# Kernel optimization log

Hardware: AMD Instinct MI355X
Metric: run time of the kernel (lower is better)

Reference implementation:

```python
import jax, jax.numpy as jnp
import numpy as np

IN_FEATURES = 4096
OUT_FEATURES = 4096
TOKENS = 8192


def setup_inputs() -> dict:
    key = jax.random.key(0)
    kx, kw, kb = jax.random.split(key, 3)
    x = jax.random.normal(kx, (TOKENS, IN_FEATURES), dtype=jnp.float32)
    # Simulate the offline quantization: a float weight quantized to 2-bit signed {-2,-1,0,1}
    w_f = jax.random.normal(kw, (OUT_FEATURES, IN_FEATURES), dtype=jnp.float32) * 0.02
    max_val = jnp.max(jnp.abs(w_f))
    scale = (max_val / 1.5 + 1e-8).astype(jnp.float32)
    weight_q = jnp.clip(jnp.round(w_f / scale), -2, 1).astype(jnp.int8)
    bias = jax.random.normal(kb, (OUT_FEATURES,), dtype=jnp.float32) * 0.01
    return {"x": x, "weight_q": weight_q, "scale": scale, "bias": bias}


def reference(x, weight_q, scale, bias):
    # Dequantize 2-bit weights then standard linear: y = x @ W^T + b
    w = weight_q.astype(jnp.float32) * scale  # [out, in]
    return jnp.einsum('ti,oi->to', x, w) + bias
```

## Files before the change

### kernel.cpp

```cpp
#include <hip/hip_runtime.h>
#include <stdint.h>

#define TOKENS 8192
#define INF    4096
#define OUTF   4096
#define NT     64

typedef __bf16 bf16x8 __attribute__((ext_vector_type(8)));
typedef float  f32x4  __attribute__((ext_vector_type(4)));
typedef unsigned short ushort_t;

__device__ __forceinline__ unsigned short f2bf(float f) {
  union { float f; unsigned int u; } v;
  v.f = f;
  unsigned int r = v.u + 0x7fffu + ((v.u >> 16) & 1u);
  return (unsigned short)(r >> 16);
}

__global__ void l2b_conv_x(const float* __restrict__ x,
                           unsigned short* __restrict__ xb, int n4) {
  int idx = blockIdx.x * blockDim.x + threadIdx.x;
  int stride = gridDim.x * blockDim.x;
  for (int i = idx; i < n4; i += stride) {
    float4 v = reinterpret_cast<const float4*>(x)[i];
    ushort4 o;
    o.x = f2bf(v.x); o.y = f2bf(v.y); o.z = f2bf(v.z); o.w = f2bf(v.w);
    reinterpret_cast<ushort4*>(xb)[i] = o;
  }
}

__global__ void l2b_conv_w(const int* __restrict__ w,
                           unsigned short* __restrict__ wb, int n4) {
  int idx = blockIdx.x * blockDim.x + threadIdx.x;
  int stride = gridDim.x * blockDim.x;
  for (int i = idx; i < n4; i += stride) {
    int4 v = reinterpret_cast<const int4*>(w)[i];
    ushort4 o;
    o.x = f2bf((float)v.x); o.y = f2bf((float)v.y);
    o.z = f2bf((float)v.z); o.w = f2bf((float)v.w);
    reinterpret_cast<ushort4*>(wb)[i] = o;
  }
}

__device__ __forceinline__ void gload_lds16(const ushort_t* g, ushort_t* l) {
  auto gp = reinterpret_cast<__attribute__((address_space(1))) unsigned int*>(
      reinterpret_cast<uintptr_t>(g));
  auto lp = reinterpret_cast<__attribute__((address_space(3))) unsigned int*>(
      reinterpret_cast<uintptr_t>(l));
  __builtin_amdgcn_global_load_lds(gp, lp, 16, 0, 0);
}

__device__ __forceinline__ bf16x8 ldsRd(const ushort_t* slot, int row, int chunk) {
  const int off = (row << 7) + ((chunk ^ (row & 7)) << 4);
  return *reinterpret_cast<const bf16x8*>(
      reinterpret_cast<const char*>(slot) + off);
}

__device__ __forceinline__ void stage_half(const ushort_t* __restrict__ src,
                                           ushort_t* slot, int wid,
                                           int ge0, int ge1) {
  gload_lds16(src + ge0, slot + wid * 512);
  gload_lds16(src + ge1, slot + 4096 + wid * 512);
}

__device__ __forceinline__ f32x4 mfma(bf16x8 a, bf16x8 b, f32x4 c) {
  return __builtin_amdgcn_mfma_f32_16x16x32_bf16(a, b, c, 0, 0, 0);
}

template <int N>
__device__ __forceinline__ void vmwait() {
  if constexpr (N == 4)      asm volatile("s_waitcnt vmcnt(4)" ::: "memory");
  else if constexpr (N == 0) asm volatile("s_waitcnt vmcnt(0)" ::: "memory");
}

#define PHASE_SYNC()                                            \
  __builtin_amdgcn_s_barrier();                                 \
  asm volatile("s_waitcnt lgkmcnt(0)" ::: "memory");            \
  __builtin_amdgcn_sched_barrier(0);                            \
  __builtin_amdgcn_s_setprio(1)

#define PHASE_END() __builtin_amdgcn_s_setprio(0)

template <int VMB, bool STG1, bool STG2>
__device__ __forceinline__ void ktile(
    const ushort_t* __restrict__ A, const ushort_t* __restrict__ B,
    int rowBlk, int colBlk, int t,
    ushort_t* rA0, ushort_t* rA1, ushort_t* rB0, ushort_t* rB1,
    ushort_t* oA1, ushort_t* oB0,
    f32x4 (&acc)[8][4], int ar, int br, int fk, int wid, int ge0, int ge1) {
  bf16x8 a[4][2], b[2][2];
#pragma unroll
  for (int m = 0; m < 4; ++m) {
    a[m][0] = ldsRd(rA0, ar + m * 16, fk);
    a[m][1] = ldsRd(rA0, ar + m * 16, 4 + fk);
  }
#pragma unroll
  for (int n = 0; n < 2; ++n) {
    b[n][0] = ldsRd(rB0, br + n * 16, fk);
    b[n][1] = ldsRd(rB0, br + n * 16, 4 + fk);
  }
  if (STG1)
    stage_half(A + (size_t)(rowBlk + 128) * INF + (t + 1) * 64, oA1, wid, ge0, ge1);
  PHASE_SYNC();
#pragma unroll
  for (int m = 0; m < 4; ++m)
#pragma unroll
    for (int n = 0; n < 2; ++n) {
      acc[m][n] = mfma(a[m][0], b[n][0], acc[m][n]);
      acc[m][n] = mfma(a[m][1], b[n][1], acc[m][n]);
    }
  PHASE_END();
  __builtin_amdgcn_s_barrier();
#pragma unroll
  for (int n = 0; n < 2; ++n) {
    b[n][0] = ldsRd(rB1, br + n * 16, fk);
    b[n][1] = ldsRd(rB1, br + n * 16, 4 + fk);
  }
  if (STG1)
    stage_half(B + (size_t)colBlk * INF + (t + 1) * 64, oB0, wid, ge0, ge1);
  PHASE_SYNC();
#pragma unroll
  for (int m = 0; m < 4; ++m)
#pragma unroll
    for (int n = 0; n < 2; ++n) {
      acc[m][2 + n] = mfma(a[m][0], b[n][0], acc[m][2 + n]);
      acc[m][2 + n] = mfma(a[m][1], b[n][1], acc[m][2 + n]);
    }
  PHASE_END();
  __builtin_amdgcn_s_barrier();
#pragma unroll
  for (int m = 0; m < 4; ++m) {
    a[m][0] = ldsRd(rA1, ar + m * 16, fk);
    a[m][1] = ldsRd(rA1, ar + m * 16, 4 + fk);
  }
  if (STG2)
    stage_half(A + (size_t)rowBlk * INF + (t + 2) * 64, rA0, wid, ge0, ge1);
  PHASE_SYNC();
#pragma unroll
  for (int m = 0; m < 4; ++m)
#pragma unroll
    for (int n = 0; n < 2; ++n) {
      acc[4 + m][2 + n] = mfma(a[m][0], b[n][0], acc[4 + m][2 + n]);
      acc[4 + m][2 + n] = mfma(a[m][1], b[n][1], acc[4 + m][2 + n]);
    }
  PHASE_END();
  __builtin_amdgcn_s_barrier();
#pragma unroll
  for (int n = 0; n < 2; ++n) {
    b[n][0] = ldsRd(rB0, br + n * 16, fk);
    b[n][1] = ldsRd(rB0, br + n * 16, 4 + fk);
  }
  if (STG2)
    stage_half(B + (size_t)(colBlk + 128) * INF + (t + 2) * 64, rB1, wid, ge0, ge1);
  PHASE_SYNC();
#pragma unroll
  for (int m = 0; m < 4; ++m)
#pragma unroll
    for (int n = 0; n < 2; ++n) {
      acc[4 + m][n] = mfma(a[m][0], b[n][0], acc[4 + m][n]);
      acc[4 + m][n] = mfma(a[m][1], b[n][1], acc[4 + m][n]);
    }
  PHASE_END();
  if (VMB >= 0) vmwait<VMB >= 0 ? VMB : 0>();
  __builtin_amdgcn_s_barrier();
}

__global__ __launch_bounds__(512, 2) void l2b_gemm8(
    const ushort_t* __restrict__ A, const ushort_t* __restrict__ B,
    const float* __restrict__ scale, const float* __restrict__ bias,
    float* __restrict__ C) {
  extern __shared__ ushort_t smem[];
  ushort_t* sA00 = smem;              ushort_t* sA01 = smem + 8192;
  ushort_t* sA10 = smem + 16384;      ushort_t* sA11 = smem + 24576;
  ushort_t* sB00 = smem + 32768;      ushort_t* sB01 = smem + 40960;
  ushort_t* sB10 = smem + 49152;      ushort_t* sB11 = smem + 57344;

  const int tid  = threadIdx.x;
  const int lane = tid & 63;
  const int wid  = tid >> 6;
  const int wm = wid >> 2, wn = wid & 3;
  const int fr = lane & 15, fk = lane >> 4;
  const int ar = wm * 64 + fr;
  const int br = wn * 32 + fr;

  const int bid = (int)blockIdx.x;
  const int idx = (bid & 7) * 64 + (bid >> 3);
  const int bm = idx >> 4, bn = idx & 15;
  const int rowBlk = bm * 256, colBlk = bn * 256;

  const int ob0 = wid * 1024 + lane * 16;
  const int ob1 = 8192 + ob0;
  const int r0 = ob0 >> 7, c0 = (ob0 >> 4) & 7;
  const int r1 = ob1 >> 7, c1 = (ob1 >> 4) & 7;
  const int ge0 = r0 * INF + ((c0 ^ (r0 & 7)) << 3);
  const int ge1 = r1 * INF + ((c1 ^ (r1 & 7)) << 3);

  stage_half(A + (size_t)rowBlk * INF,               sA00, wid, ge0, ge1);
  stage_half(B + (size_t)(colBlk + 128) * INF,       sB01, wid, ge0, ge1);
  stage_half(A + (size_t)(rowBlk + 128) * INF,       sA01, wid, ge0, ge1);
  stage_half(B + (size_t)colBlk * INF,               sB00, wid, ge0, ge1);
  stage_half(A + (size_t)rowBlk * INF + 64,          sA10, wid, ge0, ge1);
  stage_half(B + (size_t)(colBlk + 128) * INF + 64,  sB11, wid, ge0, ge1);
  asm volatile("s_waitcnt vmcnt(4)" ::: "memory");
  __builtin_amdgcn_s_barrier();

  f32x4 acc[8][4] = {};

#pragma unroll 1
  for (int i = 0; i < 31; ++i) {
    const int t = 2 * i;
    ktile<4, true, true>(A, B, rowBlk, colBlk, t,
        sA00, sA01, sB00, sB01, sA11, sB10,
        acc, ar, br, fk, wid, ge0, ge1);
    ktile<4, true, true>(A, B, rowBlk, colBlk, t + 1,
        sA10, sA11, sB10, sB11, sA01, sB00,
        acc, ar, br, fk, wid, ge0, ge1);
  }
  ktile<0, true, false>(A, B, rowBlk, colBlk, 62,
      sA00, sA01, sB00, sB01, sA11, sB10,
      acc, ar, br, fk, wid, ge0, ge1);
  ktile<-1, false, false>(A, B, rowBlk, colBlk, 63,
      sA10, sA11, sB10, sB11, sA01, sB00,
      acc, ar, br, fk, wid, ge0, ge1);

  const float s = scale[0];
#pragma unroll
  for (int ni = 0; ni < 4; ++ni) {
    const int nh = ni >> 1, n = ni & 1;
    const int col = colBlk + nh * 128 + wn * 32 + n * 16 + fr;
    const float bv = bias[col];
#pragma unroll
    for (int mi = 0; mi < 8; ++mi) {
      const int mh = mi >> 2, m = mi & 3;
      const int row = rowBlk + mh * 128 + wm * 64 + m * 16 + fk * 4;
#pragma unroll
      for (int j = 0; j < 4; ++j)
        C[(size_t)(row + j) * OUTF + col] = acc[mi][ni][j] * s + bv;
    }
  }
}

__global__ __launch_bounds__(256) void l2b_gemm(
    const ushort_t* __restrict__ A, const ushort_t* __restrict__ B,
    const float* __restrict__ scale, const float* __restrict__ bias,
    float* __restrict__ C) {
  constexpr int K = INF;
  constexpr int N = OUTF;
  __shared__ __align__(16) ushort_t ldsA[128 * 32];
  __shared__ __align__(16) ushort_t ldsB[128 * 32];
  const int tid = threadIdx.x;
  const int lane = tid & 63;
  const int wid = tid >> 6;
  const int wm = wid >> 1, wn = wid & 1;
  const int bm = blockIdx.x >> 5, bn = blockIdx.x & 31;
  const int row0 = bm * 128, col0 = bn * 128;
  const int lr = lane >> 4, lc = lane & 15;
  f32x4 acc[4][4] = {};
  for (int k0 = 0; k0 < K; k0 += 32) {
#pragma unroll
    for (int i = 0; i < 2; ++i) {
      const int idx = i * 256 + tid;
      const int r = idx >> 2;
      const int c = (idx & 3) * 8;
      ushort_t* lbaseA = ldsA + i * 2048 + wid * 512;
      ushort_t* lbaseB = ldsB + i * 2048 + wid * 512;
      gload_lds16(A + (size_t)(row0 + r) * K + (k0 + c), lbaseA);
      gload_lds16(B + (size_t)(col0 + r) * K + (k0 + c), lbaseB);
    }
    __syncthreads();
    bf16x8 af[4], bfr[4];
#pragma unroll
    for (int m = 0; m < 4; ++m)
      af[m] = *reinterpret_cast<const bf16x8*>(
          &ldsA[(wm * 64 + m * 16 + lc) * 32 + lr * 8]);
#pragma unroll
    for (int n = 0; n < 4; ++n)
      bfr[n] = *reinterpret_cast<const bf16x8*>(
          &ldsB[(wn * 64 + n * 16 + lc) * 32 + lr * 8]);
#pragma unroll
    for (int m = 0; m < 4; ++m)
#pragma unroll
      for (int n = 0; n < 4; ++n)
        acc[m][n] = mfma(af[m], bfr[n], acc[m][n]);
    __syncthreads();
  }
  const float s = scale[0];
#pragma unroll
  for (int n = 0; n < 4; ++n) {
    const int col = col0 + wn * 64 + n * 16 + lc;
    const float bv = bias[col];
#pragma unroll
    for (int m = 0; m < 4; ++m) {
      const int row = row0 + wm * 64 + m * 16 + lr * 4;
#pragma unroll
      for (int i = 0; i < 4; ++i)
        C[(size_t)(row + i) * N + col] = acc[m][n][i] * s + bv;
    }
  }
}

__global__ void l2b_naive(const float* __restrict__ x, const int* __restrict__ w,
                          const float* __restrict__ scale,
                          const float* __restrict__ bias,
                          float* __restrict__ out) {
  const int o = blockIdx.x * blockDim.x + threadIdx.x;
  if (o >= TOKENS * OUTF) return;
  const int t = o / OUTF;
  const int n = o - t * OUTF;
  const float* xr = x + (size_t)t * INF;
  const int* wr = w + (size_t)n * INF;
  float acc = 0.f;
  for (int k = 0; k < INF; ++k) acc += xr[k] * (float)wr[k];
  out[o] = acc * scale[0] + bias[n];
}

extern "C" void kernel_launch(void* const* d_in, const int* in_sizes, int n_in,
                              void* d_out, int out_size, void* d_ws, size_t ws_size,
                              hipStream_t stream) {
  const float* x     = (const float*)d_in[0];
  const int*   wq    = (const int*)d_in[1];
  const float* scale = (const float*)d_in[2];
  const float* bias  = (const float*)d_in[3];
  float* out = (float*)d_out;

  const size_t xbytes = (size_t)TOKENS * INF * 2;
  const size_t wbytes = (size_t)OUTF * INF * 2;

  if (ws_size >= xbytes + wbytes) {
    unsigned short* xb = (unsigned short*)d_ws;
    unsigned short* wb = (unsigned short*)((char*)d_ws + xbytes);
    l2b_conv_x<<<2048, 256, 0, stream>>>(x, xb, TOKENS * INF / 4);
    l2b_conv_w<<<2048, 256, 0, stream>>>(wq, wb, OUTF * INF / 4);

    hipError_t e = hipFuncSetAttribute(
        reinterpret_cast<const void*>(l2b_gemm8),
        hipFuncAttributeMaxDynamicSharedMemorySize, 131072);
    if (e == hipSuccess) {
      l2b_gemm8<<<dim3((TOKENS / 256) * (OUTF / 256)), 512, 131072, stream>>>(
          xb, wb, scale, bias, out);
    } else {
      l2b_gemm<<<dim3((TOKENS / 128) * (OUTF / 128)), 256, 0, stream>>>(
          xb, wb, scale, bias, out);
    }
  } else {
    l2b_naive<<<(TOKENS * OUTF + 255) / 256, 256, 0, stream>>>(
        x, wq, scale, bias, out);
  }
}
```

Baseline: 263.6 us.

## Prefetch next k-tile fragments into registers and reorder LDS staging phases

Restructures the 4-phase k-tile loop so that each tile's A0/B0 fragments are read from LDS at the end of the previous tile and carried in registers. The LDS staging order is reshuffled to match, and lgkmcnt waits become partial instead of full. The XOR swizzle changes from a per-row chunk XOR to a single-bit XOR on bit 5, and launch bounds drop from 2 to 1 block per CU. The goal is to hide LDS read latency behind MFMA work, at the cost of more registers and lower occupancy, and the new swizzle may bring LDS bank conflicts.

Measured after the change: 708.8 us. 169% more time.

```diff
diff --git a/kernel.cpp b/kernel.cpp
--- a/kernel.cpp
+++ b/kernel.cpp
@@ -50,8 +50,11 @@
   __builtin_amdgcn_global_load_lds(gp, lp, 16, 0, 0);
 }
 
-__device__ __forceinline__ bf16x8 ldsRd(const ushort_t* slot, int row, int chunk) {
-  const int off = (row << 7) + ((chunk ^ (row & 7)) << 4);
+__device__ __forceinline__ int swz(int b) { return b ^ (((b >> 9) & 1) << 5); }
+
+__device__ __forceinline__ bf16x8 ldsRd(const ushort_t* slot, int row, int colb) {
+  int off = (row << 7) | colb;
+  off ^= ((off >> 9) & 1) << 5;
   return *reinterpret_cast<const bf16x8*>(
       reinterpret_cast<const char*>(slot) + off);
 }
@@ -67,113 +70,117 @@
   return __builtin_amdgcn_mfma_f32_16x16x32_bf16(a, b, c, 0, 0, 0);
 }
 
-template <int N>
-__device__ __forceinline__ void vmwait() {
-  if constexpr (N == 4)      asm volatile("s_waitcnt vmcnt(4)" ::: "memory");
-  else if constexpr (N == 0) asm volatile("s_waitcnt vmcnt(0)" ::: "memory");
-}
-
-#define PHASE_SYNC()                                            \
-  __builtin_amdgcn_s_barrier();                                 \
-  asm volatile("s_waitcnt lgkmcnt(0)" ::: "memory");            \
-  __builtin_amdgcn_sched_barrier(0);                            \
-  __builtin_amdgcn_s_setprio(1)
-
-#define PHASE_END() __builtin_amdgcn_s_setprio(0)
-
-template <int VMB, bool STG1, bool STG2>
+#define LGKM(n)                                                \
+  asm volatile("s_waitcnt lgkmcnt(" #n ")" ::: "memory");      \
+  __builtin_amdgcn_sched_barrier(0)
+
+#define BAR() __builtin_amdgcn_s_barrier()
+
+template <int VMB, bool STG_B1, bool STG_T2, bool PRER>
 __device__ __forceinline__ void ktile(
     const ushort_t* __restrict__ A, const ushort_t* __restrict__ B,
     int rowBlk, int colBlk, int t,
-    ushort_t* rA0, ushort_t* rA1, ushort_t* rB0, ushort_t* rB1,
-    ushort_t* oA1, ushort_t* oB0,
+    const ushort_t* rA0, const ushort_t* rA1,
+    const ushort_t* rB0, const ushort_t* rB1,
+    ushort_t* sB1n,
+    ushort_t* sB0p, ushort_t* sA0p, ushort_t* sA1p,
+    const ushort_t* nA0, const ushort_t* nB0,
+    bf16x8 (&a0)[4][2], bf16x8 (&a1)[4][2],
+    bf16x8 (&b0c)[2][2], bf16x8 (&b0n)[2][2],
     f32x4 (&acc)[8][4], int ar, int br, int fk, int wid, int ge0, int ge1) {
-  bf16x8 a[4][2], b[2][2];
+  const int cb = fk * 16;
+  bf16x8 b1[2][2];
+#pragma unroll
+  for (int n = 0; n < 2; ++n) {
+    b1[n][0] = ldsRd(rB1, br + n * 16, cb);
+    b1[n][1] = ldsRd(rB1, br + n * 16, 64 + cb);
+  }
+  if (STG_B1)
+    stage_half(B + (size_t)(colBlk + 128) * INF + (t + 1) * 64, sB1n, wid, ge0, ge1);
+  BAR();
+  LGKM(4);
+  __builtin_amdgcn_s_setprio(1);
+#pragma unroll
+  for (int m = 0; m < 4; ++m)
+#pragma unroll
+    for (int n = 0; n < 2; ++n) {
+      acc[m][n] = mfma(a0[m][0], b0c[n][0], acc[m][n]);
+      acc[m][n] = mfma(a0[m][1], b0c[n][1], acc[m][n]);
+    }
+  __builtin_amdgcn_s_setprio(0);
+  BAR();
 #pragma unroll
   for (int m = 0; m < 4; ++m) {
-    a[m][0] = ldsRd(rA0, ar + m * 16, fk);
-    a[m][1] = ldsRd(rA0, ar + m * 16, 4 + fk);
-  }
-#pragma unroll
-  for (int n = 0; n < 2; ++n) {
-    b[n][0] = ldsRd(rB0, br + n * 16, fk);
-    b[n][1] = ldsRd(rB0, br + n * 16, 4 + fk);
-  }
-  if (STG1)
-    stage_half(A + (size_t)(rowBlk + 128) * INF + (t + 1) * 64, oA1, wid, ge0, ge1);
-  PHASE_SYNC();
+    a1[m][0] = ldsRd(rA1, ar + m * 16, cb);
+    a1[m][1] = ldsRd(rA1, ar + m * 16, 64 + cb);
+  }
+  if (STG_T2)
+    stage_half(B + (size_t)colBlk * INF + (t + 2) * 64, sB0p, wid, ge0, ge1);
+  BAR();
+  LGKM(8);
+  __builtin_amdgcn_s_setprio(1);
 #pragma unroll
   for (int m = 0; m < 4; ++m)
 #pragma unroll
     for (int n = 0; n < 2; ++n) {
-      acc[m][n] = mfma(a[m][0], b[n][0], acc[m][n]);
-      acc[m][n] = mfma(a[m][1], b[n][1], acc[m][n]);
-    }
-  PHASE_END();
-  __builtin_amdgcn_s_barrier();
-#pragma unroll
-  for (int n = 0; n < 2; ++n) {
-    b[n][0] = ldsRd(rB1, br + n * 16, fk);
-    b[n][1] = ldsRd(rB1, br + n * 16, 4 + fk);
-  }
-  if (STG1)
-    stage_half(B + (size_t)colBlk * INF + (t + 1) * 64, oB0, wid, ge0, ge1);
-  PHASE_SYNC();
+      acc[m][2 + n] = mfma(a0[m][0], b1[n][0], acc[m][2 + n]);
+      acc[m][2 + n] = mfma(a0[m][1], b1[n][1], acc[m][2 + n]);
+    }
+  __builtin_amdgcn_s_setprio(0);
+  BAR();
+  if (STG_T2)
+    stage_half(A + (size_t)rowBlk * INF + (t + 2) * 64, sA0p, wid, ge0, ge1);
+  BAR();
+  LGKM(0);
+  __builtin_amdgcn_s_setprio(1);
 #pragma unroll
   for (int m = 0; m < 4; ++m)
 #pragma unroll
     for (int n = 0; n < 2; ++n) {
-      acc[m][2 + n] = mfma(a[m][0], b[n][0], acc[m][2 + n]);
-      acc[m][2 + n] = mfma(a[m][1], b[n][1], acc[m][2 + n]);
-    }
-  PHASE_END();
-  __builtin_amdgcn_s_barrier();
-#pragma unroll
-  for (int m = 0; m < 4; ++m) {
-    a[m][0] = ldsRd(rA1, ar + m * 16, fk);
-    a[m][1] = ldsRd(rA1, ar + m * 16, 4 + fk);
-  }
-  if (STG2)
-    stage_half(A + (size_t)rowBlk * INF + (t + 2) * 64, rA0, wid, ge0, ge1);
-  PHASE_SYNC();
+      acc[4 + m][2 + n] = mfma(a1[m][0], b1[n][0], acc[4 + m][2 + n]);
+      acc[4 + m][2 + n] = mfma(a1[m][1], b1[n][1], acc[4 + m][2 + n]);
+    }
+  __builtin_amdgcn_s_setprio(0);
+  if (VMB == 4) asm volatile("s_waitcnt vmcnt(4)" ::: "memory");
+  if (VMB == 0) asm volatile("s_waitcnt vmcnt(0)" ::: "memory");
+  BAR();
+  if (PRER) {
+#pragma unroll
+    for (int m = 0; m < 4; ++m) {
+      a0[m][0] = ldsRd(nA0, ar + m * 16, cb);
+      a0[m][1] = ldsRd(nA0, ar + m * 16, 64 + cb);
+    }
+#pragma unroll
+    for (int n = 0; n < 2; ++n) {
+      b0n[n][0] = ldsRd(nB0, br + n * 16, cb);
+      b0n[n][1] = ldsRd(nB0, br + n * 16, 64 + cb);
+    }
+  }
+  if (STG_T2)
+    stage_half(A + (size_t)(rowBlk + 128) * INF + (t + 2) * 64, sA1p, wid, ge0, ge1);
+  BAR();
+  __builtin_amdgcn_sched_barrier(0);
+  __builtin_amdgcn_s_setprio(1);
 #pragma unroll
   for (int m = 0; m < 4; ++m)
 #pragma unroll
     for (int n = 0; n < 2; ++n) {
-      acc[4 + m][2 + n] = mfma(a[m][0], b[n][0], acc[4 + m][2 + n]);
-      acc[4 + m][2 + n] = mfma(a[m][1], b[n][1], acc[4 + m][2 + n]);
-    }
-  PHASE_END();
-  __builtin_amdgcn_s_barrier();
-#pragma unroll
-  for (int n = 0; n < 2; ++n) {
-    b[n][0] = ldsRd(rB0, br + n * 16, fk);
-    b[n][1] = ldsRd(rB0, br + n * 16, 4 + fk);
-  }
-  if (STG2)
-    stage_half(B + (size_t)(colBlk + 128) * INF + (t + 2) * 64, rB1, wid, ge0, ge1);
-  PHASE_SYNC();
-#pragma unroll
-  for (int m = 0; m < 4; ++m)
-#pragma unroll
-    for (int n = 0; n < 2; ++n) {
-      acc[4 + m][n] = mfma(a[m][0], b[n][0], acc[4 + m][n]);
-      acc[4 + m][n] = mfma(a[m][1], b[n][1], acc[4 + m][n]);
-    }
-  PHASE_END();
-  if (VMB >= 0) vmwait<VMB >= 0 ? VMB : 0>();
-  __builtin_amdgcn_s_barrier();
-}
-
-__global__ __launch_bounds__(512, 2) void l2b_gemm8(
+      acc[4 + m][n] = mfma(a1[m][0], b0c[n][0], acc[4 + m][n]);
+      acc[4 + m][n] = mfma(a1[m][1], b0c[n][1], acc[4 + m][n]);
+    }
+  __builtin_amdgcn_s_setprio(0);
+  BAR();
+}
+
+__global__ __launch_bounds__(512, 1) void l2b_gemm8(
     const ushort_t* __restrict__ A, const ushort_t* __restrict__ B,
     const float* __restrict__ scale, const float* __restrict__ bias,
     float* __restrict__ C) {
   extern __shared__ ushort_t smem[];
-  ushort_t* sA00 = smem;              ushort_t* sA01 = smem + 8192;
-  ushort_t* sA10 = smem + 16384;      ushort_t* sA11 = smem + 24576;
-  ushort_t* sB00 = smem + 32768;      ushort_t* sB01 = smem + 40960;
-  ushort_t* sB10 = smem + 49152;      ushort_t* sB11 = smem + 57344;
+  ushort_t* sA0[2] = { smem,          smem + 8192  };
+  ushort_t* sA1[2] = { smem + 16384,  smem + 24576 };
+  ushort_t* sB0[2] = { smem + 32768,  smem + 40960 };
+  ushort_t* sB1[2] = { smem + 49152,  smem + 57344 };
 
   const int tid  = threadIdx.x;
   const int lane = tid & 63;
@@ -190,38 +197,62 @@
 
   const int ob0 = wid * 1024 + lane * 16;
   const int ob1 = 8192 + ob0;
-  const int r0 = ob0 >> 7, c0 = (ob0 >> 4) & 7;
-  const int r1 = ob1 >> 7, c1 = (ob1 >> 4) & 7;
-  const int ge0 = r0 * INF + ((c0 ^ (r0 & 7)) << 3);
-  const int ge1 = r1 * INF + ((c1 ^ (r1 & 7)) << 3);
-
-  stage_half(A + (size_t)rowBlk * INF,               sA00, wid, ge0, ge1);
-  stage_half(B + (size_t)(colBlk + 128) * INF,       sB01, wid, ge0, ge1);
-  stage_half(A + (size_t)(rowBlk + 128) * INF,       sA01, wid, ge0, ge1);
-  stage_half(B + (size_t)colBlk * INF,               sB00, wid, ge0, ge1);
-  stage_half(A + (size_t)rowBlk * INF + 64,          sA10, wid, ge0, ge1);
-  stage_half(B + (size_t)(colBlk + 128) * INF + 64,  sB11, wid, ge0, ge1);
+  const int p0 = swz(ob0), p1 = swz(ob1);
+  const int ge0 = (p0 >> 7) * INF + ((p0 & 127) >> 1);
+  const int ge1 = (p1 >> 7) * INF + ((p1 & 127) >> 1);
+
+  stage_half(A + (size_t)rowBlk * INF,              sA0[0], wid, ge0, ge1);
+  stage_half(A + (size_t)(rowBlk + 128) * INF,      sA1[0], wid, ge0, ge1);
+  stage_half(B + (size_t)colBlk * INF,              sB0[0], wid, ge0, ge1);
+  stage_half(B + (size_t)(colBlk + 128) * INF,      sB1[0], wid, ge0, ge1);
+  stage_half(B + (size_t)colBlk * INF + 64,         sB0[1], wid, ge0, ge1);
+  stage_half(A + (size_t)rowBlk * INF + 64,         sA0[1], wid, ge0, ge1);
   asm volatile("s_waitcnt vmcnt(4)" ::: "memory");
-  __builtin_amdgcn_s_barrier();
+  BAR();
+
+  bf16x8 a0[4][2], a1[4][2], b0A[2][2], b0B[2][2];
+  {
+    const int cb = fk * 16;
+#pragma unroll
+    for (int m = 0; m < 4; ++m) {
+      a0[m][0] = ldsRd(sA0[0], ar + m * 16, cb);
+      a0[m][1] = ldsRd(sA0[0], ar + m * 16, 64 + cb);
+    }
+#pragma unroll
+    for (int n = 0; n < 2; ++n) {
+      b0A[n][0] = ldsRd(sB0[0], br + n * 16, cb);
+      b0A[n][1] = ldsRd(sB0[0], br + n * 16, 64 + cb);
+    }
+  }
+  stage_half(A + (size_t)(rowBlk + 128) * INF + 64, sA1[1], wid, ge0, ge1);
+  BAR();
 
   f32x4 acc[8][4] = {};
 
 #pragma unroll 1
   for (int i = 0; i < 31; ++i) {
     const int t = 2 * i;
-    ktile<4, true, true>(A, B, rowBlk, colBlk, t,
-        sA00, sA01, sB00, sB01, sA11, sB10,
-        acc, ar, br, fk, wid, ge0, ge1);
-    ktile<4, true, true>(A, B, rowBlk, colBlk, t + 1,
-        sA10, sA11, sB10, sB11, sA01, sB00,
-        acc, ar, br, fk, wid, ge0, ge1);
-  }
-  ktile<0, true, false>(A, B, rowBlk, colBlk, 62,
-      sA00, sA01, sB00, sB01, sA11, sB10,
-      acc, ar, br, fk, wid, ge0, ge1);
-  ktile<-1, false, false>(A, B, rowBlk, colBlk, 63,
-      sA10, sA11, sB10, sB11, sA01, sB00,
-      acc, ar, br, fk, wid, ge0, ge1);
+    ktile<4, true, true, true>(A, B, rowBlk, colBlk, t,
+        sA0[0], sA1[0], sB0[0], sB1[0],
+        sB1[1], sB0[0], sA0[0], sA1[0],
+        sA0[1], sB0[1],
+        a0, a1, b0A, b0B, acc, ar, br, fk, wid, ge0, ge1);
+    ktile<4, true, true, true>(A, B, rowBlk, colBlk, t + 1,
+        sA0[1], sA1[1], sB0[1], sB1[1],
+        sB1[0], sB0[1], sA0[1], sA1[1],
+        sA0[0], sB0[0],
+        a0, a1, b0B, b0A, acc, ar, br, fk, wid, ge0, ge1);
+  }
+  ktile<0, true, false, true>(A, B, rowBlk, colBlk, 62,
+      sA0[0], sA1[0], sB0[0], sB1[0],
+      sB1[1], sB0[0], sA0[0], sA1[0],
+      sA0[1], sB0[1],
+      a0, a1, b0A, b0B, acc, ar, br, fk, wid, ge0, ge1);
+  ktile<-1, false, false, false>(A, B, rowBlk, colBlk, 63,
+      sA0[1], sA1[1], sB0[1], sB1[1],
+      sB1[0], sB0[1], sA0[1], sA1[1],
+      sA0[0], sB0[0],
+      a0, a1, b0B, b0A, acc, ar, br, fk, wid, ge0, ge1);
 
   const float s = scale[0];
 #pragma unroll
```
